# Performance work log

Hardware: AMD Instinct MI355X
Metric: run time of the kernel (lower is better)

## Reference

```python
import jax, jax.numpy as jnp
import numpy as np

N = 2048

def setup_inputs() -> dict:
    key = jax.random.key(0)
    k0, k1, k2, k3 = jax.random.split(key, 4)
    return {
        "input": jax.random.normal(k0, (N, N), dtype=jnp.float32),
        "weight1": jax.random.normal(k1, (N, N), dtype=jnp.float32),
        "weight2": jax.random.normal(k2, (N, N), dtype=jnp.float32),
        "weight3": jax.random.normal(k3, (N, N), dtype=jnp.float32),
    }

def reference(input, weight1, weight2, weight3):
    # Faithful translation of the torch DAG (duplicate mm kept: t4 == t2,
    # so t8 is mathematically zero, but we preserve the original math).
    t1 = input @ weight1
    t2 = input @ weight2
    t3 = weight3 @ weight3
    t4 = input @ weight2
    t5 = t1 * weight1
    t6 = (t5 @ input) * weight1
    t7 = t1 * t2 + t1 + t3
    t8 = t2 - t4
    t9 = t7 * t8 + t6 * t3
    t11 = t3 * t9
    t12 = t3 * (t1 @ input) * t6
    t13 = t7 + t11
    t14 = t8 + t12
    t15 = t13 + t14
    return t15
```

## Files before the change

kernel.cpp:

```cpp
#include <hip/hip_runtime.h>
#include <hip/hip_bf16.h>
#include <stdint.h>

#define NN 2048
#define BK 32

typedef __bf16 bf16;
typedef __bf16 bf16x8 __attribute__((ext_vector_type(8)));
typedef __bf16 bf16x4 __attribute__((ext_vector_type(4)));
typedef float f32x4 __attribute__((ext_vector_type(4)));

__device__ __forceinline__ void async_copy16(bf16* lds, const bf16* g) {
    __builtin_amdgcn_global_load_lds(
        (const __attribute__((address_space(1))) unsigned int*)g,
        (__attribute__((address_space(3))) unsigned int*)lds,
        16, 0, 0);
}

#define WAIT_VM(n) asm volatile("s_waitcnt vmcnt(" #n ")" ::: "memory")
#define BAR()                                  \
    do {                                       \
        asm volatile("" ::: "memory");         \
        __builtin_amdgcn_s_barrier();          \
        asm volatile("" ::: "memory");         \
    } while (0)

struct CastArgs {
    const float* in[4];
    bf16*        outT[4];
    bf16*        outN[4];
};

__global__ __launch_bounds__(256) void transpose_cast_kernel(CastArgs args) {
    const float* __restrict__ in = args.in[blockIdx.z];
    bf16* __restrict__ outT      = args.outT[blockIdx.z];
    bf16* __restrict__ outN      = args.outN[blockIdx.z];
    __shared__ float tile[64][65];
    const int bx = blockIdx.x * 64;
    const int by = blockIdx.y * 64;
    const int t  = threadIdx.x;
    const int tc = t & 15, tr = t >> 4;
#pragma unroll
    for (int p = 0; p < 4; ++p) {
        const int r = tr + p * 16;
        const float4 v = *(const float4*)&in[(size_t)(by + r) * NN + bx + tc * 4];
        tile[r][tc * 4 + 0] = v.x; tile[r][tc * 4 + 1] = v.y;
        tile[r][tc * 4 + 2] = v.z; tile[r][tc * 4 + 3] = v.w;
        if (outN) {
            bf16x4 b = {(bf16)v.x, (bf16)v.y, (bf16)v.z, (bf16)v.w};
            *(bf16x4*)&outN[(size_t)(by + r) * NN + bx + tc * 4] = b;
        }
    }
    __syncthreads();
    const int cc = t >> 2, e = t & 3;
#pragma unroll
    for (int u = 0; u < 2; ++u) {
        const int r0 = e * 16 + u * 8;
        bf16x8 b;
#pragma unroll
        for (int i = 0; i < 8; ++i) b[i] = (bf16)tile[r0 + i][cc];
        *(bf16x8*)&outT[(size_t)(bx + cc) * NN + by + r0] = b;
    }
}

struct Gemm3Args {
    const bf16*  A[3];
    const bf16*  Bt[3];
    float*       C[3];
    const float* W1;
    bf16*        M1bf;
    bf16*        B1bf;
};

__global__ __launch_bounds__(256) void gemm3_kernel(Gemm3Args args) {
    const bf16* __restrict__ A  = args.A[blockIdx.z];
    const bf16* __restrict__ Bt = args.Bt[blockIdx.z];
    float* __restrict__ C       = args.C[blockIdx.z];

    __shared__ bf16 As0[128 * BK], As1[128 * BK], As2[128 * BK];
    __shared__ bf16 Bs0[128 * BK], Bs1[128 * BK], Bs2[128 * BK];

    const int t  = threadIdx.x;
    const int bm = blockIdx.x * 128;
    const int bn = blockIdx.y * 128;

    const int row0 = t >> 2;
    const int qp   = t & 3;
    const int col0 = ((qp ^ ((row0 >> 1) & 3)) << 3);
    const int off0 = t * 8;

    const bf16* gA0 = A  + (size_t)(bm + row0) * NN + col0;
    const bf16* gB0 = Bt + (size_t)(bn + row0) * NN + col0;

    const int wave = t >> 6;
    const int lane = t & 63;
    const int wm   = (wave >> 1) * 64;
    const int wn   = (wave & 1) * 64;
    const int lrow = lane & 15;
    const int q    = lane >> 4;
    const int qe   = (q ^ ((lrow >> 1) & 3)) << 3;

    f32x4 acc[4][4];
#pragma unroll
    for (int i = 0; i < 4; ++i)
#pragma unroll
        for (int j = 0; j < 4; ++j) acc[i][j] = (f32x4){0.f, 0.f, 0.f, 0.f};

    auto issue = [&](bf16* As, bf16* Bs, int kt) {
        const int kof = kt * BK;
        async_copy16(&As[off0],           gA0 + kof);
        async_copy16(&As[off0 + 64 * BK], gA0 + (size_t)64 * NN + kof);
        async_copy16(&Bs[off0],           gB0 + kof);
        async_copy16(&Bs[off0 + 64 * BK], gB0 + (size_t)64 * NN + kof);
    };
    auto compute = [&](const bf16* As, const bf16* Bs) {
        bf16x8 af[4], bfr[4];
#pragma unroll
        for (int i = 0; i < 4; ++i)
            af[i] = *(const bf16x8*)&As[(wm + i * 16 + lrow) * BK + qe];
#pragma unroll
        for (int j = 0; j < 4; ++j)
            bfr[j] = *(const bf16x8*)&Bs[(wn + j * 16 + lrow) * BK + qe];
#pragma unroll
        for (int i = 0; i < 4; ++i)
#pragma unroll
            for (int j = 0; j < 4; ++j)
                acc[i][j] = __builtin_amdgcn_mfma_f32_16x16x32_bf16(
                    af[i], bfr[j], acc[i][j], 0, 0, 0);
    };

    issue(As0, Bs0, 0);
    issue(As1, Bs1, 1);
#pragma unroll 1
    for (int kt = 0; kt < 60; kt += 3) {
        issue(As2, Bs2, kt + 2); WAIT_VM(8); BAR(); compute(As0, Bs0); BAR();
        issue(As0, Bs0, kt + 3); WAIT_VM(8); BAR(); compute(As1, Bs1); BAR();
        issue(As1, Bs1, kt + 4); WAIT_VM(8); BAR(); compute(As2, Bs2); BAR();
    }
    issue(As2, Bs2, 62); WAIT_VM(8); BAR(); compute(As0, Bs0); BAR();
    issue(As0, Bs0, 63); WAIT_VM(8); BAR(); compute(As1, Bs1); BAR();
    WAIT_VM(4); BAR(); compute(As2, Bs2); BAR();
    WAIT_VM(0); BAR(); compute(As0, Bs0);

    const int z = blockIdx.z;
#pragma unroll
    for (int i = 0; i < 4; ++i)
#pragma unroll
        for (int j = 0; j < 4; ++j)
#pragma unroll
            for (int r = 0; r < 4; ++r) {
                const size_t idx = (size_t)(bm + wm + i * 16 + q * 4 + r) * NN +
                                   (bn + wn + j * 16 + lrow);
                const float v = acc[i][j][r];
                C[idx] = v;
                if (z == 0) {
                    const float w = args.W1[idx];
                    args.M1bf[idx] = (bf16)v;
                    args.B1bf[idx] = (bf16)(v * w);
                }
            }
}

struct Gemm2Args {
    const bf16*  M1bf;
    const bf16*  B1bf;
    const bf16*  At;
    const float* M1;
    const float* M3;
    const float* W1;
    float*       out;
};

__global__ __launch_bounds__(256) void gemm2_fused_kernel(Gemm2Args args) {
    __shared__ bf16 A50[128 * BK], A51[128 * BK], A52[128 * BK];
    __shared__ bf16 A40[128 * BK], A41[128 * BK], A42[128 * BK];
    __shared__ bf16 Bs0[64 * BK],  Bs1[64 * BK],  Bs2[64 * BK];

    const int t  = threadIdx.x;
    const int bm = blockIdx.x * 128;
    const int bn = blockIdx.y * 64;

    const int row0 = t >> 2;
    const int qp   = t & 3;
    const int col0 = ((qp ^ ((row0 >> 1) & 3)) << 3);
    const int off0 = t * 8;

    const bf16* g5 = args.M1bf + (size_t)(bm + row0) * NN + col0;
    const bf16* g4 = args.B1bf + (size_t)(bm + row0) * NN + col0;
    const bf16* gB = args.At   + (size_t)(bn + row0) * NN + col0;

    const int wave = t >> 6;
    const int lane = t & 63;
    const int wm   = (wave >> 1) * 64;
    const int wn   = (wave & 1) * 32;
    const int lrow = lane & 15;
    const int q    = lane >> 4;
    const int qe   = (q ^ ((lrow >> 1) & 3)) << 3;

    f32x4 acc5[4][2], acc4[4][2];
#pragma unroll
    for (int i = 0; i < 4; ++i)
#pragma unroll
        for (int j = 0; j < 2; ++j) {
            acc5[i][j] = (f32x4){0.f, 0.f, 0.f, 0.f};
            acc4[i][j] = (f32x4){0.f, 0.f, 0.f, 0.f};
        }

    auto issue = [&](bf16* A5, bf16* A4, bf16* Bs, int kt) {
        const int kof = kt * BK;
        async_copy16(&A5[off0],           g5 + kof);
        async_copy16(&A5[off0 + 64 * BK], g5 + (size_t)64 * NN + kof);
        async_copy16(&A4[off0],           g4 + kof);
        async_copy16(&A4[off0 + 64 * BK], g4 + (size_t)64 * NN + kof);
        async_copy16(&Bs[off0],           gB + kof);
    };
    auto compute = [&](const bf16* A5, const bf16* A4, const bf16* Bs) {
        bf16x8 a5[4], a4[4], bfr[2];
#pragma unroll
        for (int i = 0; i < 4; ++i) {
            a5[i] = *(const bf16x8*)&A5[(wm + i * 16 + lrow) * BK + qe];
            a4[i] = *(const bf16x8*)&A4[(wm + i * 16 + lrow) * BK + qe];
        }
#pragma unroll
        for (int j = 0; j < 2; ++j)
            bfr[j] = *(const bf16x8*)&Bs[(wn + j * 16 + lrow) * BK + qe];
#pragma unroll
        for (int i = 0; i < 4; ++i)
#pragma unroll
            for (int j = 0; j < 2; ++j) {
                acc5[i][j] = __builtin_amdgcn_mfma_f32_16x16x32_bf16(
                    a5[i], bfr[j], acc5[i][j], 0, 0, 0);
                acc4[i][j] = __builtin_amdgcn_mfma_f32_16x16x32_bf16(
                    a4[i], bfr[j], acc4[i][j], 0, 0, 0);
            }
    };

    issue(A50, A40, Bs0, 0);
    issue(A51, A41, Bs1, 1);
#pragma unroll 1
    for (int kt = 0; kt < 60; kt += 3) {
        issue(A52, A42, Bs2, kt + 2); WAIT_VM(10); BAR(); compute(A50, A40, Bs0); BAR();
        issue(A50, A40, Bs0, kt + 3); WAIT_VM(10); BAR(); compute(A51, A41, Bs1); BAR();
        issue(A51, A41, Bs1, kt + 4); WAIT_VM(10); BAR(); compute(A52, A42, Bs2); BAR();
    }
    issue(A52, A42, Bs2, 62); WAIT_VM(10); BAR(); compute(A50, A40, Bs0); BAR();
    issue(A50, A40, Bs0, 63); WAIT_VM(10); BAR(); compute(A51, A41, Bs1); BAR();
    WAIT_VM(5); BAR(); compute(A52, A42, Bs2); BAR();
    WAIT_VM(0); BAR(); compute(A50, A40, Bs0);

#pragma unroll
    for (int i = 0; i < 4; ++i)
#pragma unroll
        for (int j = 0; j < 2; ++j)
#pragma unroll
            for (int r = 0; r < 4; ++r) {
                const size_t idx = (size_t)(bm + wm + i * 16 + q * 4 + r) * NN +
                                   (bn + wn + j * 16 + lrow);
                const float m5 = acc5[i][j][r];
                const float m4 = acc4[i][j][r];
                const float m1 = args.M1[idx];
                const float m3 = args.M3[idx];
                const float w1 = args.W1[idx];
                const float m2 = args.out[idx];
                args.out[idx] =
                    m1 * m2 + m1 + m3 + m3 * (m4 * w1) * (m3 + m5);
            }
}

extern "C" void kernel_launch(void* const* d_in, const int* in_sizes, int n_in,
                              void* d_out, int out_size, void* d_ws, size_t ws_size,
                              hipStream_t stream) {
    const float* A  = (const float*)d_in[0];
    const float* W1 = (const float*)d_in[1];
    const float* W2 = (const float*)d_in[2];
    const float* W3 = (const float*)d_in[3];
    float* out = (float*)d_out;

    const size_t P = (size_t)NN * NN;
    char* ws = (char*)d_ws;

    bf16* Abf  = (bf16*)ws;
    bf16* At   = Abf + P;
    bf16* W1t  = At + P;
    bf16* W2t  = W1t + P;
    bf16* W3bf = W2t + P;
    bf16* W3t  = W3bf + P;
    bf16* M1bf = W3t + P;
    bf16* B1bf = M1bf + P;
    float* M1  = (float*)(B1bf + P);
    float* M3  = M1 + P;

    CastArgs ca;
    ca.in[0] = A;  ca.outT[0] = At;  ca.outN[0] = Abf;
    ca.in[1] = W1; ca.outT[1] = W1t; ca.outN[1] = nullptr;
    ca.in[2] = W2; ca.outT[2] = W2t; ca.outN[2] = nullptr;
    ca.in[3] = W3; ca.outT[3] = W3t; ca.outN[3] = W3bf;
    transpose_cast_kernel<<<dim3(NN / 64, NN / 64, 4), 256, 0, stream>>>(ca);

    Gemm3Args g3;
    g3.A[0] = Abf;  g3.Bt[0] = W1t; g3.C[0] = M1;
    g3.A[1] = Abf;  g3.Bt[1] = W2t; g3.C[1] = out;
    g3.A[2] = W3bf; g3.Bt[2] = W3t; g3.C[2] = M3;
    g3.W1 = W1; g3.M1bf = M1bf; g3.B1bf = B1bf;
    gemm3_kernel<<<dim3(NN / 128, NN / 128, 3), 256, 0, stream>>>(g3);

    Gemm2Args g2;
    g2.M1bf = M1bf; g2.B1bf = B1bf; g2.At = At;
    g2.M1 = M1; g2.M3 = M3; g2.W1 = W1; g2.out = out;
    gemm2_fused_kernel<<<dim3(NN / 128, NN / 64), 256, 0, stream>>>(g2);
}
```

Measured before the change: 258.6 us.

## Retile second dual GEMM to 64x64 with BK=64, split M1 epilogue into separate kernel

The second-stage dual GEMM moves to 64x64 output tiles with a K-step of 64, double buffering instead of triple, an XOR swizzle over 8 column blocks, and a launch bound asking for 3 blocks per CU. This gives 1024 blocks instead of 512 and fewer barrier rounds, aiming at better occupancy and latency hiding. The bf16 M1 and M1*W1 conversions leave the batched GEMM epilogue for a separate vectorized elementwise kernel, which removes per-element W1 loads and the branch from the z==0 GEMM slice at the cost of one extra launch and a reread of M1. The transpose kernel's write-out pass is also remapped so adjacent threads write contiguous 16-byte chunks.

Result: faster. 238.0 us (-7.9%).

```diff
diff --git a/kernel.cpp b/kernel.cpp
--- a/kernel.cpp
+++ b/kernel.cpp
@@ -39,40 +39,37 @@
     const int bx = blockIdx.x * 64;
     const int by = blockIdx.y * 64;
     const int t  = threadIdx.x;
-    const int tc = t & 15, tr = t >> 4;
+    const int c4 = (t & 15) * 4, r0 = t >> 4;
 #pragma unroll
     for (int p = 0; p < 4; ++p) {
-        const int r = tr + p * 16;
-        const float4 v = *(const float4*)&in[(size_t)(by + r) * NN + bx + tc * 4];
-        tile[r][tc * 4 + 0] = v.x; tile[r][tc * 4 + 1] = v.y;
-        tile[r][tc * 4 + 2] = v.z; tile[r][tc * 4 + 3] = v.w;
+        const int r = r0 + p * 16;
+        const float4 v = *(const float4*)&in[(size_t)(by + r) * NN + bx + c4];
+        tile[r][c4 + 0] = v.x; tile[r][c4 + 1] = v.y;
+        tile[r][c4 + 2] = v.z; tile[r][c4 + 3] = v.w;
         if (outN) {
             bf16x4 b = {(bf16)v.x, (bf16)v.y, (bf16)v.z, (bf16)v.w};
-            *(bf16x4*)&outN[(size_t)(by + r) * NN + bx + tc * 4] = b;
+            *(bf16x4*)&outN[(size_t)(by + r) * NN + bx + c4] = b;
         }
     }
     __syncthreads();
-    const int cc = t >> 2, e = t & 3;
-#pragma unroll
-    for (int u = 0; u < 2; ++u) {
-        const int r0 = e * 16 + u * 8;
+    const int cc8 = (t & 7) * 8, rw0 = t >> 3;
+#pragma unroll
+    for (int p = 0; p < 2; ++p) {
+        const int rw = rw0 + p * 32;
         bf16x8 b;
 #pragma unroll
-        for (int i = 0; i < 8; ++i) b[i] = (bf16)tile[r0 + i][cc];
-        *(bf16x8*)&outT[(size_t)(bx + cc) * NN + by + r0] = b;
+        for (int i = 0; i < 8; ++i) b[i] = (bf16)tile[cc8 + i][rw];
+        *(bf16x8*)&outT[(size_t)(bx + rw) * NN + by + cc8] = b;
     }
 }
 
-struct Gemm3Args {
-    const bf16*  A[3];
-    const bf16*  Bt[3];
-    float*       C[3];
-    const float* W1;
-    bf16*        M1bf;
-    bf16*        B1bf;
+struct GemmArgs {
+    const bf16* A[3];
+    const bf16* Bt[3];
+    float*      C[3];
 };
 
-__global__ __launch_bounds__(256) void gemm3_kernel(Gemm3Args args) {
+__global__ __launch_bounds__(256) void gemm_bt_batched(GemmArgs args) {
     const bf16* __restrict__ A  = args.A[blockIdx.z];
     const bf16* __restrict__ Bt = args.Bt[blockIdx.z];
     float* __restrict__ C       = args.C[blockIdx.z];
@@ -142,23 +139,28 @@
     WAIT_VM(4); BAR(); compute(As2, Bs2); BAR();
     WAIT_VM(0); BAR(); compute(As0, Bs0);
 
-    const int z = blockIdx.z;
 #pragma unroll
     for (int i = 0; i < 4; ++i)
 #pragma unroll
         for (int j = 0; j < 4; ++j)
 #pragma unroll
-            for (int r = 0; r < 4; ++r) {
-                const size_t idx = (size_t)(bm + wm + i * 16 + q * 4 + r) * NN +
-                                   (bn + wn + j * 16 + lrow);
-                const float v = acc[i][j][r];
-                C[idx] = v;
-                if (z == 0) {
-                    const float w = args.W1[idx];
-                    args.M1bf[idx] = (bf16)v;
-                    args.B1bf[idx] = (bf16)(v * w);
-                }
-            }
+            for (int r = 0; r < 4; ++r)
+                C[(size_t)(bm + wm + i * 16 + q * 4 + r) * NN +
+                  (bn + wn + j * 16 + lrow)] = acc[i][j][r];
+}
+
+__global__ void post_m1_kernel(const float* __restrict__ M1,
+                               const float* __restrict__ W1,
+                               bf16* __restrict__ M1bf,
+                               bf16* __restrict__ B1bf) {
+    const size_t i = ((size_t)blockIdx.x * 256 + threadIdx.x) * 4;
+    const float4 m = *(const float4*)&M1[i];
+    const float4 w = *(const float4*)&W1[i];
+    bf16x4 mb = {(bf16)m.x, (bf16)m.y, (bf16)m.z, (bf16)m.w};
+    bf16x4 bb = {(bf16)(m.x * w.x), (bf16)(m.y * w.y),
+                 (bf16)(m.z * w.z), (bf16)(m.w * w.w)};
+    *(bf16x4*)&M1bf[i] = mb;
+    *(bf16x4*)&B1bf[i] = bb;
 }
 
 struct Gemm2Args {
@@ -171,18 +173,18 @@
     float*       out;
 };
 
-__global__ __launch_bounds__(256) void gemm2_fused_kernel(Gemm2Args args) {
-    __shared__ bf16 A50[128 * BK], A51[128 * BK], A52[128 * BK];
-    __shared__ bf16 A40[128 * BK], A41[128 * BK], A42[128 * BK];
-    __shared__ bf16 Bs0[64 * BK],  Bs1[64 * BK],  Bs2[64 * BK];
+__global__ __launch_bounds__(256, 3) void p2_dual_kernel(Gemm2Args args) {
+    __shared__ bf16 A50[64 * 64], A51[64 * 64];
+    __shared__ bf16 A40[64 * 64], A41[64 * 64];
+    __shared__ bf16 Bs0[64 * 64], Bs1[64 * 64];
 
     const int t  = threadIdx.x;
-    const int bm = blockIdx.x * 128;
+    const int bm = blockIdx.x * 64;
     const int bn = blockIdx.y * 64;
 
-    const int row0 = t >> 2;
-    const int qp   = t & 3;
-    const int col0 = ((qp ^ ((row0 >> 1) & 3)) << 3);
+    const int row0 = t >> 3;
+    const int cbp  = t & 7;
+    const int col0 = ((cbp ^ (row0 & 7)) << 3);
     const int off0 = t * 8;
 
     const bf16* g5 = args.M1bf + (size_t)(bm + row0) * NN + col0;
@@ -191,15 +193,15 @@
 
     const int wave = t >> 6;
     const int lane = t & 63;
-    const int wm   = (wave >> 1) * 64;
+    const int wm   = (wave >> 1) * 32;
     const int wn   = (wave & 1) * 32;
     const int lrow = lane & 15;
     const int q    = lane >> 4;
-    const int qe   = (q ^ ((lrow >> 1) & 3)) << 3;
-
-    f32x4 acc5[4][2], acc4[4][2];
-#pragma unroll
-    for (int i = 0; i < 4; ++i)
+    const int l7   = lrow & 7;
+
+    f32x4 acc5[2][2], acc4[2][2];
+#pragma unroll
+    for (int i = 0; i < 2; ++i)
 #pragma unroll
         for (int j = 0; j < 2; ++j) {
             acc5[i][j] = (f32x4){0.f, 0.f, 0.f, 0.f};
@@ -207,49 +209,55 @@
         }
 
     auto issue = [&](bf16* A5, bf16* A4, bf16* Bs, int kt) {
-        const int kof = kt * BK;
-        async_copy16(&A5[off0],           g5 + kof);
-        async_copy16(&A5[off0 + 64 * BK], g5 + (size_t)64 * NN + kof);
-        async_copy16(&A4[off0],           g4 + kof);
-        async_copy16(&A4[off0 + 64 * BK], g4 + (size_t)64 * NN + kof);
-        async_copy16(&Bs[off0],           gB + kof);
+        const int kof = kt * 64;
+        async_copy16(&A5[off0],        g5 + kof);
+        async_copy16(&A5[off0 + 2048], g5 + (size_t)32 * NN + kof);
+        async_copy16(&A4[off0],        g4 + kof);
+        async_copy16(&A4[off0 + 2048], g4 + (size_t)32 * NN + kof);
+        async_copy16(&Bs[off0],        gB + kof);
+        async_copy16(&Bs[off0 + 2048], gB + (size_t)32 * NN + kof);
     };
     auto compute = [&](const bf16* A5, const bf16* A4, const bf16* Bs) {
-        bf16x8 a5[4], a4[4], bfr[2];
-#pragma unroll
-        for (int i = 0; i < 4; ++i) {
-            a5[i] = *(const bf16x8*)&A5[(wm + i * 16 + lrow) * BK + qe];
-            a4[i] = *(const bf16x8*)&A4[(wm + i * 16 + lrow) * BK + qe];
+#pragma unroll
+        for (int ks = 0; ks < 2; ++ks) {
+            const int ce = (((ks << 2) + q) ^ l7) << 3;
+            bf16x8 a5[2], a4[2], bfr[2];
+#pragma unroll
+            for (int i = 0; i < 2; ++i) {
+                const int ra = wm + i * 16 + lrow;
+                a5[i] = *(const bf16x8*)&A5[ra * 64 + ce];
+                a4[i] = *(const bf16x8*)&A4[ra * 64 + ce];
+            }
+#pragma unroll
+            for (int j = 0; j < 2; ++j)
+                bfr[j] = *(const bf16x8*)&Bs[(wn + j * 16 + lrow) * 64 + ce];
+#pragma unroll
+            for (int i = 0; i < 2; ++i)
+#pragma unroll
+                for (int j = 0; j < 2; ++j) {
+                    acc5[i][j] = __builtin_amdgcn_mfma_f32_16x16x32_bf16(
+                        a5[i], bfr[j], acc5[i][j], 0, 0, 0);
+                    acc4[i][j] = __builtin_amdgcn_mfma_f32_16x16x32_bf16(
+                        a4[i], bfr[j], acc4[i][j], 0, 0, 0);
+                }
         }
-#pragma unroll
-        for (int j = 0; j < 2; ++j)
-            bfr[j] = *(const bf16x8*)&Bs[(wn + j * 16 + lrow) * BK + qe];
-#pragma unroll
-        for (int i = 0; i < 4; ++i)
-#pragma unroll
-            for (int j = 0; j < 2; ++j) {
-                acc5[i][j] = __builtin_amdgcn_mfma_f32_16x16x32_bf16(
-                    a5[i], bfr[j], acc5[i][j], 0, 0, 0);
-                acc4[i][j] = __builtin_amdgcn_mfma_f32_16x16x32_bf16(
-                    a4[i], bfr[j], acc4[i][j], 0, 0, 0);
-            }
     };
 
     issue(A50, A40, Bs0, 0);
-    issue(A51, A41, Bs1, 1);
 #pragma unroll 1
-    for (int kt = 0; kt < 60; kt += 3) {
-        issue(A52, A42, Bs2, kt + 2); WAIT_VM(10); BAR(); compute(A50, A40, Bs0); BAR();
-        issue(A50, A40, Bs0, kt + 3); WAIT_VM(10); BAR(); compute(A51, A41, Bs1); BAR();
-        issue(A51, A41, Bs1, kt + 4); WAIT_VM(10); BAR(); compute(A52, A42, Bs2); BAR();
+    for (int kt = 0; kt < 30; kt += 2) {
+        issue(A51, A41, Bs1, kt + 1); WAIT_VM(6); BAR();
+        compute(A50, A40, Bs0); BAR();
+        issue(A50, A40, Bs0, kt + 2); WAIT_VM(6); BAR();
+        compute(A51, A41, Bs1); BAR();
     }
-    issue(A52, A42, Bs2, 62); WAIT_VM(10); BAR(); compute(A50, A40, Bs0); BAR();
-    issue(A50, A40, Bs0, 63); WAIT_VM(10); BAR(); compute(A51, A41, Bs1); BAR();
-    WAIT_VM(5); BAR(); compute(A52, A42, Bs2); BAR();
-    WAIT_VM(0); BAR(); compute(A50, A40, Bs0);
-
-#pragma unroll
-    for (int i = 0; i < 4; ++i)
+    issue(A51, A41, Bs1, 31); WAIT_VM(6); BAR();
+    compute(A50, A40, Bs0); BAR();
+    WAIT_VM(0); BAR();
+    compute(A51, A41, Bs1);
+
+#pragma unroll
+    for (int i = 0; i < 2; ++i)
 #pragma unroll
         for (int j = 0; j < 2; ++j)
 #pragma unroll
@@ -297,15 +305,16 @@
     ca.in[3] = W3; ca.outT[3] = W3t; ca.outN[3] = W3bf;
     transpose_cast_kernel<<<dim3(NN / 64, NN / 64, 4), 256, 0, stream>>>(ca);
 
-    Gemm3Args g3;
+    GemmArgs g3;
     g3.A[0] = Abf;  g3.Bt[0] = W1t; g3.C[0] = M1;
     g3.A[1] = Abf;  g3.Bt[1] = W2t; g3.C[1] = out;
     g3.A[2] = W3bf; g3.Bt[2] = W3t; g3.C[2] = M3;
-    g3.W1 = W1; g3.M1bf = M1bf; g3.B1bf = B1bf;
-    gemm3_kernel<<<dim3(NN / 128, NN / 128, 3), 256, 0, stream>>>(g3);
+    gemm_bt_batched<<<dim3(NN / 128, NN / 128, 3), 256, 0, stream>>>(g3);
+
+    post_m1_kernel<<<(P / 4) / 256, 256, 0, stream>>>(M1, W1, M1bf, B1bf);
 
     Gemm2Args g2;
     g2.M1bf = M1bf; g2.B1bf = B1bf; g2.At = At;
     g2.M1 = M1; g2.M3 = M3; g2.W1 = W1; g2.out = out;
-    gemm2_fused_kernel<<<dim3(NN / 128, NN / 64), 256, 0, stream>>>(g2);
-}
+    p2_dual_kernel<<<dim3(NN / 64, NN / 64), 256, 0, stream>>>(g2);
+}
```
